# Kernel optimization log

Hardware: AMD Instinct MI355X
Metric: run time of the kernel (lower is better)

## Reference

```python
import jax, jax.numpy as jnp
import numpy as np

B, T, D = 2, 2048, 1024
H = 16
HD = D // H  # head_dim = 64 (kv_rank == embed_dim)
INT4_MIN, INT4_MAX = -8.0, 7.0


def _int4_quant_dequant(x):
    # per-token amax over last dim (head_dim), as in INT4Quantizer with 4-D input
    amax = jnp.max(jnp.abs(x), axis=-1, keepdims=True)
    amax = jnp.maximum(amax, 1e-5)
    scale = amax / 7.0
    q = jnp.clip(jnp.round(x / scale), INT4_MIN, INT4_MAX)  # stored as int8 in cache
    return q * scale


def setup_inputs() -> dict:
    key = jax.random.key(0)
    ks = jax.random.split(key, 11)
    s = 1.0 / np.sqrt(D)
    return {
        "query": jax.random.normal(ks[0], (B, T, D), jnp.float32),
        "key": jax.random.normal(ks[1], (B, T, D), jnp.float32),
        "value": jax.random.normal(ks[2], (B, T, D), jnp.float32),
        "Wq": jax.random.normal(ks[3], (D, D), jnp.float32) * s,
        "bq": jnp.zeros((D,), jnp.float32),
        "Wk": jax.random.normal(ks[4], (D, D), jnp.float32) * s,
        "bk": jnp.zeros((D,), jnp.float32),
        "Wv": jax.random.normal(ks[5], (D, D), jnp.float32) * s,
        "bv": jnp.zeros((D,), jnp.float32),
        "Wo": jax.random.normal(ks[6], (D, D), jnp.float32) * s,
        "bo": jnp.zeros((D,), jnp.float32),
    }


def reference(query, key, value, Wq, bq, Wk, bk, Wv, bv, Wo, bo):
    # projections (nn.Linear: x @ W.T + b)
    q = query @ Wq.T + bq
    k = key @ Wk.T + bk
    v = value @ Wv.T + bv
    # (B, T, D) -> (B, H, T, HD)
    q = q.reshape(B, T, H, HD).transpose(0, 2, 1, 3)
    k = k.reshape(B, T, H, HD).transpose(0, 2, 1, 3)
    v = v.reshape(B, T, H, HD).transpose(0, 2, 1, 3)
    # INT4 quantized KV cache update (use_cache=True): quantize -> scatter into
    # fresh cache -> dequantize the just-written block == quant/dequant of k, v
    k = _int4_quant_dequant(k)
    v = _int4_quant_dequant(v)
    # attention
    scale = HD ** (-0.5)
    attn = jnp.einsum("bhqd,bhkd->bhqk", q, k) * scale
    attn = jax.nn.softmax(attn.astype(jnp.float32), axis=-1).astype(query.dtype)
    out = jnp.einsum("bhqk,bhkd->bhqd", attn, v)
    out = out.transpose(0, 2, 1, 3).reshape(B, T, D)
    out = out @ Wo.T + bo
    return out
```

## Files before the change

### kernel.cpp

```cpp
#include <hip/hip_runtime.h>

typedef unsigned short u16;
typedef unsigned int u32;
typedef float f32x4 __attribute__((ext_vector_type(4)));
typedef float f32x16 __attribute__((ext_vector_type(16)));
typedef short s16x8 __attribute__((ext_vector_type(8)));
typedef u16 u16x8 __attribute__((ext_vector_type(8)));
typedef u16 u16x4 __attribute__((ext_vector_type(4)));
typedef u32 u32x4 __attribute__((ext_vector_type(4)));
typedef _Float16 h16x8 __attribute__((ext_vector_type(8)));
typedef _Float16 h16x2 __attribute__((ext_vector_type(2)));

#define B_ 2
#define T_ 2048
#define H_ 16
#define D_ 1024
#define HD_ 64
#define NTOK (B_*T_)

#define QSCALE 0.18033688011112042f

__device__ __forceinline__ u16 f2b(float f){
  u32 u = __float_as_uint(f);
  return (u16)((u + 0x7fffu + ((u>>16)&1u)) >> 16);
}
__device__ __forceinline__ float b2f(u16 h){ return __uint_as_float(((u32)h)<<16); }

__device__ __forceinline__ void gload_lds16(const u16* g, u16* s){
  __builtin_amdgcn_global_load_lds((const __attribute__((address_space(1))) void*)g,
                                   (__attribute__((address_space(3))) void*)s, 16, 0, 0);
}

template<int ROWS, int WAVES>
__device__ __forceinline__ void stage_tile(const u16* __restrict__ g, size_t ldg,
                                           u16* s, int tid){
  const int w = tid>>6, l = tid&63;
  const int rw = ROWS/WAVES;
  #pragma unroll
  for (int i=0;i<ROWS/(WAVES*8);i++){
    int r0 = w*rw + i*8;
    int r  = r0 + (l>>3);
    int u  = (l&7) ^ (r&7);
    gload_lds16(g + (size_t)r*ldg + (size_t)u*8, s + r0*64);
  }
}

__device__ __forceinline__ u16x8 read_frag(const u16* s, int r, int kk, int l){
  int u = (kk<<2) | (l>>4);
  int phys = u ^ (r&7);
  return *(const u16x8*)(s + r*64 + phys*8);
}
__device__ __forceinline__ u16x8 rfragT(const u16* s, int r, int ks, int hi){
  int phys = (ks*2 + hi) ^ (r&7);
  return *(const u16x8*)(s + r*64 + phys*8);
}

__device__ __forceinline__ void stage_tile32(const u16* __restrict__ g, size_t ldg,
                                             u16* s, int tid){
  const int w = tid>>6, l = tid&63;
  int r0 = w*16;
  int r  = r0 + (l>>2);
  int v  = (l&3) ^ ((r>>1)&3);
  gload_lds16(g + (size_t)r*ldg + (size_t)v*8, s + r0*32);
}
__device__ __forceinline__ u16x8 read_frag32(const u16* s, int r, int l){
  int phys = (l>>4) ^ ((r>>1)&3);
  return *(const u16x8*)(s + r*32 + phys*8);
}

__device__ __forceinline__ f32x4 mfma16_f16(u16x8 a, u16x8 b, f32x4 c){
  return __builtin_amdgcn_mfma_f32_16x16x32_f16(
      __builtin_bit_cast(h16x8,a), __builtin_bit_cast(h16x8,b), c, 0,0,0);
}
__device__ __forceinline__ f32x4 mfma16_bf16(u16x8 a, u16x8 b, f32x4 c){
  return __builtin_amdgcn_mfma_f32_16x16x32_bf16(
      __builtin_bit_cast(s16x8,a), __builtin_bit_cast(s16x8,b), c, 0,0,0);
}
__device__ __forceinline__ f32x16 mfma32_f16(u16x8 a, u16x8 b, f32x16 c){
  return __builtin_amdgcn_mfma_f32_32x32x16_f16(
      __builtin_bit_cast(h16x8,a), __builtin_bit_cast(h16x8,b), c, 0,0,0);
}

__device__ __forceinline__ float ex2(float x){
#if __has_builtin(__builtin_amdgcn_exp2f)
  return __builtin_amdgcn_exp2f(x);
#else
  return exp2f(x);
#endif
}
__device__ __forceinline__ u32 pk2(float a, float b){
  u16 x = __builtin_bit_cast(u16, (_Float16)a);
  u16 y = __builtin_bit_cast(u16, (_Float16)b);
  return (u32)x | ((u32)y<<16);
}
__device__ __forceinline__ u32 pkrtz(float a, float b){
#if __has_builtin(__builtin_amdgcn_cvt_pkrtz)
  auto r = __builtin_amdgcn_cvt_pkrtz(a, b);
  return __builtin_bit_cast(u32, r);
#else
  return pk2(a, b);
#endif
}

__device__ __forceinline__ void split_bf4(const float* in, u16* hi, u16* lo, int i){
  f32x4 v = ((const f32x4*)in)[i];
  u16x4 h, lw;
  #pragma unroll
  for (int j=0;j<4;j++){
    u16 hb = f2b(v[j]);
    h[j] = hb;
    lw[j] = f2b(v[j] - b2f(hb));
  }
  ((u16x4*)hi)[i] = h;
  ((u16x4*)lo)[i] = lw;
}
__device__ __forceinline__ void split_h4(const float* in, u16* out, int i){
  f32x4 v = ((const f32x4*)in)[i];
  u16x4 o;
  #pragma unroll
  for (int j=0;j<4;j++){
    _Float16 t = (_Float16)v[j];
    o[j] = __builtin_bit_cast(u16, t);
  }
  ((u16x4*)out)[i] = o;
}

__global__ void split_inputs_kernel(const float* __restrict__ q, const float* __restrict__ k,
                                    const float* __restrict__ v,
                                    u16* __restrict__ qh, u16* __restrict__ khi, u16* __restrict__ klo,
                                    u16* __restrict__ vhi, u16* __restrict__ vlo){
  int i = blockIdx.x*256 + threadIdx.x;
  int which = blockIdx.y;
  if (which==0)      split_h4 (q, qh, i);
  else if (which==1) split_bf4(k, khi, klo, i);
  else               split_bf4(v, vhi, vlo, i);
}

__global__ void split_weights_kernel(const float* __restrict__ wq, const float* __restrict__ wk,
                                     const float* __restrict__ wv, const float* __restrict__ wo,
                                     u16* __restrict__ wqh, u16* __restrict__ wkh, u16* __restrict__ wkl,
                                     u16* __restrict__ wvh, u16* __restrict__ wvl, u16* __restrict__ woh){
  int i = blockIdx.x*256 + threadIdx.x;
  int which = blockIdx.y;
  if (which==0)      split_h4 (wq, wqh, i);
  else if (which==1) split_bf4(wk, wkh, wkl, i);
  else if (which==2) split_bf4(wv, wvh, wvl, i);
  else               split_h4 (wo, woh, i);
}

template<int F16OUT>
__global__ __launch_bounds__(512)
void gemm1(const u16* __restrict__ Ah, const u16* __restrict__ Wh,
           const float* __restrict__ bias, void* __restrict__ Cout, float oscale)
{
  __shared__ u16 sA[2][128*64];
  __shared__ u16 sW[2][64*64];
  const int tid = threadIdx.x, l = tid&63, l15 = l&15, g = l>>4, w = tid>>6;
  const int wm = w>>1, wn = w&1;
  const int bm = blockIdx.x, bn = blockIdx.y;
  const u16* A0 = Ah + (size_t)bm*128*D_;
  const u16* W0 = Wh + (size_t)bn*64*D_;
  f32x4 acc[2][2] = {};

  stage_tile<128,8>(A0, D_, sA[0], tid);
  stage_tile<64 ,8>(W0, D_, sW[0], tid);
  __syncthreads();
  for (int t=0; t<D_/64; ++t){
    const int cur = t&1;
    if (t+1 < D_/64){
      stage_tile<128,8>(A0 + (t+1)*64, D_, sA[cur^1], tid);
      stage_tile<64 ,8>(W0 + (t+1)*64, D_, sW[cur^1], tid);
    }
    #pragma unroll
    for (int kk=0;kk<2;kk++){
      u16x8 af[2], wf[2];
      #pragma unroll
      for (int fm=0;fm<2;fm++) af[fm] = read_frag(sA[cur], wm*32+fm*16+l15, kk, l);
      #pragma unroll
      for (int fn=0;fn<2;fn++) wf[fn] = read_frag(sW[cur], wn*32+fn*16+l15, kk, l);
      #pragma unroll
      for (int fm=0;fm<2;fm++)
        #pragma unroll
        for (int fn=0;fn<2;fn++)
          acc[fm][fn] = mfma16_f16(af[fm], wf[fn], acc[fm][fn]);
    }
    __syncthreads();
  }

  #pragma unroll
  for (int fn=0; fn<2; fn++){
    int col = bn*64 + wn*32 + fn*16 + l15;
    float bv = bias[col];
    #pragma unroll
    for (int fm=0; fm<2; fm++){
      int r0 = bm*128 + wm*32 + fm*16 + g*4;
      #pragma unroll
      for (int j=0;j<4;j++){
        float v = (acc[fm][fn][j] + bv) * oscale;
        if constexpr (F16OUT){
          ((_Float16*)Cout)[(size_t)(r0+j)*D_ + col] = (_Float16)v;
        } else {
          ((float*)Cout)[(size_t)(r0+j)*D_ + col] = v;
        }
      }
    }
  }
}

template<int QMODE>
__global__ __launch_bounds__(512)
void gemm3_quant(const u16* __restrict__ Ah, const u16* __restrict__ Al,
                 const u16* __restrict__ Wh, const u16* __restrict__ Wl,
                 const float* __restrict__ bias, u16* __restrict__ Out)
{
  extern __shared__ u16 sm[];
  const int tid = threadIdx.x, l = tid&63, w = tid>>6, l15 = l&15, g = l>>4;
  const int wm = w>>1, wn = w&1;
  const int bm = blockIdx.x, bn = blockIdx.y;
  const u16* A0 = Ah + (size_t)bm*128*D_;
  const u16* A1 = Al + (size_t)bm*128*D_;
  const u16* W0 = Wh + (size_t)bn*128*D_;
  const u16* W1 = Wl + (size_t)bn*128*D_;
  constexpr int TS = 128*32;
  f32x4 acc[2][4] = {};

  auto stage = [&](int buf, int t){
    u16* base = sm + buf*4*TS;
    stage_tile32(A0 + t*32, D_, base       , tid);
    stage_tile32(A1 + t*32, D_, base +   TS, tid);
    stage_tile32(W0 + t*32, D_, base + 2*TS, tid);
    stage_tile32(W1 + t*32, D_, base + 3*TS, tid);
  };
  stage(0,0);
  __syncthreads();
  for (int t=0; t<D_/32; ++t){
    const int cur = t&1;
    if (t+1 < D_/32) stage(cur^1, t+1);
    const u16* base = sm + cur*4*TS;
    u16x8 ahh[2], ahl[2], whh[4], whl[4];
    #pragma unroll
    for (int fm=0;fm<2;fm++){
      ahh[fm] = read_frag32(base     , wm*32+fm*16+l15, l);
      ahl[fm] = read_frag32(base+  TS, wm*32+fm*16+l15, l);
    }
    #pragma unroll
    for (int fn=0;fn<4;fn++){
      whh[fn] = read_frag32(base+2*TS, wn*64+fn*16+l15, l);
      whl[fn] = read_frag32(base+3*TS, wn*64+fn*16+l15, l);
    }
    #pragma unroll
    for (int fm=0;fm<2;fm++)
      #pragma unroll
      for (int fn=0;fn<4;fn++){
        acc[fm][fn] = mfma16_bf16(ahh[fm], whh[fn], acc[fm][fn]);
        acc[fm][fn] = mfma16_bf16(ahh[fm], whl[fn], acc[fm][fn]);
        acc[fm][fn] = mfma16_bf16(ahl[fm], whh[fn], acc[fm][fn]);
      }
    __syncthreads();
  }

  #pragma unroll
  for (int fn=0;fn<4;fn++){
    float bv = bias[bn*128 + wn*64 + fn*16 + l15];
    #pragma unroll
    for (int fm=0;fm<2;fm++)
      #pragma unroll
      for (int j=0;j<4;j++) acc[fm][fn][j] += bv;
  }

  u16 (*sdq)[136] = (u16(*)[136])sm;
  #pragma unroll
  for (int fm=0;fm<2;fm++)
    #pragma unroll
    for (int j=0;j<4;j++){
      float a = 0.f;
      #pragma unroll
      for (int fn=0;fn<4;fn++) a = fmaxf(a, fabsf(acc[fm][fn][j]));
      a = fmaxf(a, __shfl_xor(a,1)); a = fmaxf(a, __shfl_xor(a,2));
      a = fmaxf(a, __shfl_xor(a,4)); a = fmaxf(a, __shfl_xor(a,8));
      a = fmaxf(a, 1e-5f);
      float scale = a / 7.0f;
      int row = wm*32 + fm*16 + g*4 + j;
      #pragma unroll
      for (int fn=0;fn<4;fn++){
        float q = rintf(acc[fm][fn][j] / scale);
        q = fminf(fmaxf(q, -8.f), 7.f);
        _Float16 dq = (_Float16)(q * scale);
        int col = wn*64 + fn*16 + l15;
        if (QMODE==1) sdq[row][col] = __builtin_bit_cast(u16, dq);
        else          sdq[col][row] = __builtin_bit_cast(u16, dq);
      }
    }
  __syncthreads();

  if (QMODE==1){
    int r = tid>>2, seg = tid&3;
    u16* dst = Out + (size_t)(bm*128 + r)*D_ + bn*128 + seg*32;
    #pragma unroll
    for (int i=0;i<4;i++)
      *(u16x8*)(dst + i*8) = *(const u16x8*)&sdq[r][seg*32 + i*8];
  } else {
    int cc = tid>>2, seg = tid&3;
    int hh = 2*bn + (cc>>6), dd = cc&63, b = bm>>4;
    u16* dst = Out + ((size_t)((b*H_+hh)*HD_ + dd))*T_ + (bm&15)*128 + seg*32;
    #pragma unroll
    for (int i=0;i<4;i++)
      *(u16x8*)(dst + i*8) = *(const u16x8*)&sdq[cc][seg*32 + i*8];
  }
}

__global__ __launch_bounds__(256, 4)
void attn_kernel(const _Float16* __restrict__ Qp, const u16* __restrict__ Kdq,
                 const u16* __restrict__ Vt, float* __restrict__ po,
                 float* __restrict__ pl)
{
  __shared__ u16 sK[2][64*64];
  __shared__ u16 sV[2][64*64];
  const int tid = threadIdx.x, l = tid&63, c = l&31, hi = l>>5, w = tid>>6;
  const int dsp = blockIdx.x;
  const int xcd = dsp & 7, slot = dsp >> 3;
  const int bh = xcd*4 + (slot>>5);
  const int rem = slot & 31;
  const int qb = rem >> 1, sp = rem & 1;
  const int b = bh>>4, h = bh&15;
  const int off = 4*hi;

  u16x8 qf[4];
  {
    const u16* qrow = (const u16*)Qp + (size_t)(b*T_ + qb*128 + w*32 + c)*D_ + h*HD_;
    #pragma unroll
    for (int ks=0;ks<4;ks++)
      qf[ks] = *(const u16x8*)(qrow + ks*16 + hi*8);
  }

  f32x16 o0 = {}, o1 = {};
  float lsp = 0.f;

  const u16* Kb = Kdq + (size_t)(b*T_ + sp*1024)*D_ + h*HD_;
  const u16* Vb = Vt  + (size_t)(bh*HD_)*T_ + sp*1024;

  stage_tile<64,4>(Kb, D_, sK[0], tid);
  stage_tile<64,4>(Vb, T_, sV[0], tid);
  __syncthreads();

  for (int kt=0; kt<16; kt++){
    const int cur = kt&1;
    if (kt+1 < 16){
      stage_tile<64,4>(Kb + (size_t)((kt+1)*64)*D_, D_, sK[cur^1], tid);
      stage_tile<64,4>(Vb + (kt+1)*64,              T_, sV[cur^1], tid);
    }
    const u16* sKc = sK[cur];
    const u16* sVc = sV[cur];

    #pragma unroll
    for (int kb=0;kb<2;kb++){
      f32x16 s = {};
      #pragma unroll
      for (int ks=0;ks<4;ks++){
        u16x8 kf = rfragT(sKc, kb*32 + c, ks, hi);
        s = mfma32_f16(kf, qf[ks], s);
      }
      u16x8 vfr[2][2];
      #pragma unroll
      for (int vr=0;vr<2;vr++){
        int rv = vr*32 + c;
        int rx = rv & 7;
        const u16* vb = sVc + rv*64 + off;
        #pragma unroll
        for (int part=0;part<2;part++){
          int u0 = 4*kb + 2*part;
          u16x4 lo4 = *(const u16x4*)(vb + ((u0  ) ^ rx)*8);
          u16x4 hi4 = *(const u16x4*)(vb + ((u0+1) ^ rx)*8);
          struct { u16x4 a, b; } t{lo4, hi4};
          vfr[vr][part] = __builtin_bit_cast(u16x8, t);
        }
      }
      float p[16];
      #pragma unroll
      for (int r=0;r<16;r++) p[r] = ex2(s[r]);
      {
        float t0 = (p[0]+p[1]) + (p[2]+p[3]);
        float t1 = (p[4]+p[5]) + (p[6]+p[7]);
        float t2 = (p[8]+p[9]) + (p[10]+p[11]);
        float t3 = (p[12]+p[13]) + (p[14]+p[15]);
        lsp += (t0+t1) + (t2+t3);
      }
      u32x4 pw0 = { pkrtz(p[0],p[1]),  pkrtz(p[2],p[3]),
                    pkrtz(p[4],p[5]),  pkrtz(p[6],p[7]) };
      u32x4 pw1 = { pkrtz(p[8],p[9]),  pkrtz(p[10],p[11]),
                    pkrtz(p[12],p[13]),pkrtz(p[14],p[15]) };
      u16x8 pa0 = __builtin_bit_cast(u16x8, pw0);
      u16x8 pa1 = __builtin_bit_cast(u16x8, pw1);
      o0 = mfma32_f16(pa0, vfr[0][0], o0);
      o0 = mfma32_f16(pa1, vfr[0][1], o0);
      o1 = mfma32_f16(pa0, vfr[1][0], o1);
      o1 = mfma32_f16(pa1, vfr[1][1], o1);
    }
    __syncthreads();
  }

  float lt = lsp + __shfl_xor(lsp, 32);
  if (hi == 0) pl[(size_t)(sp*32 + bh)*T_ + qb*128 + w*32 + c] = lt;

  float* pob = po + ((size_t)(sp*32 + bh)*T_ + qb*128 + w*32)*HD_;
  #pragma unroll
  for (int r=0;r<16;r++){
    int crow = (r&3) + 8*(r>>2) + 4*hi;
    pob[crow*HD_ + c]      = o0[r];
    pob[crow*HD_ + 32 + c] = o1[r];
  }
}

__global__ __launch_bounds__(256)
void combine_kernel(const float* __restrict__ po, const float* __restrict__ pl,
                    u16* __restrict__ Ao)
{
  int i = blockIdx.x*256 + threadIdx.x;
  int d4 = (i & 15) * 4;
  int t  = (i >> 4) & (T_-1);
  int bh = i >> 15;
  size_t r0 = ((size_t)bh*T_ + t);
  f32x4 a = *(const f32x4*)(po + r0*HD_ + d4);
  f32x4 b = *(const f32x4*)(po + (r0 + (size_t)32*T_)*HD_ + d4);
  float lt = pl[r0] + pl[r0 + (size_t)32*T_];
  float rl = 1.0f / lt;
  u16x4 o;
  #pragma unroll
  for (int j=0;j<4;j++)
    o[j] = __builtin_bit_cast(u16, (_Float16)((a[j]+b[j])*rl));
  int bb = bh>>4, hh = bh&15;
  *(u16x4*)(Ao + ((size_t)(bb*T_ + t))*D_ + hh*HD_ + d4) = o;
}

extern "C" void kernel_launch(void* const* d_in, const int* in_sizes, int n_in,
                              void* d_out, int out_size, void* d_ws, size_t ws_size,
                              hipStream_t stream)
{
  (void)in_sizes; (void)n_in; (void)out_size; (void)ws_size;
  const float* query = (const float*)d_in[0];
  const float* key   = (const float*)d_in[1];
  const float* value = (const float*)d_in[2];
  const float* Wq = (const float*)d_in[3];
  const float* bq = (const float*)d_in[4];
  const float* Wk = (const float*)d_in[5];
  const float* bk = (const float*)d_in[6];
  const float* Wv = (const float*)d_in[7];
  const float* bv = (const float*)d_in[8];
  const float* Wo = (const float*)d_in[9];
  const float* bo = (const float*)d_in[10];
  float* out = (float*)d_out;

  char* p = (char*)d_ws;
  auto take = [&](size_t n){ char* r = p; p += (n + 255) & ~(size_t)255; return r; };
  const size_t big = (size_t)NTOK*D_*2;
  const size_t wsz = (size_t)D_*D_*2;

  u16* q_h  = (u16*)take(big);
  u16* khi  = (u16*)take(big);  u16* klo = (u16*)take(big);
  u16* vhi  = (u16*)take(big);  u16* vlo = (u16*)take(big);
  u16* wq_h = (u16*)take(wsz);
  u16* wkh  = (u16*)take(wsz);  u16* wkl = (u16*)take(wsz);
  u16* wvh  = (u16*)take(wsz);  u16* wvl = (u16*)take(wsz);
  u16* wo_h = (u16*)take(wsz);
  u16*  Qp  = (u16*)take(big);
  u16*  Kdq = (u16*)take(big);
  u16*  Vtp = (u16*)take(big);
  u16*  Ao  = (u16*)take(big);

  float* po = (float*)khi;
  float* pl = (float*)wq_h;

  split_inputs_kernel <<<dim3(NTOK*D_/4/256, 3), 256, 0, stream>>>(
      query, key, value, q_h, khi, klo, vhi, vlo);
  split_weights_kernel<<<dim3(D_*D_/4/256, 4), 256, 0, stream>>>(
      Wq, Wk, Wv, Wo, wq_h, wkh, wkl, wvh, wvl, wo_h);

  gemm1<1><<<dim3(32,16), 512, 0, stream>>>(q_h, wq_h, bq, Qp, QSCALE);
  gemm3_quant<1><<<dim3(32,8), 512, 64*1024, stream>>>(khi, klo, wkh, wkl, bk, Kdq);
  gemm3_quant<2><<<dim3(32,8), 512, 64*1024, stream>>>(vhi, vlo, wvh, wvl, bv, Vtp);

  attn_kernel<<<1024, 256, 0, stream>>>((const _Float16*)Qp, Kdq, Vtp, po, pl);
  combine_kernel<<<4096, 256, 0, stream>>>(po, pl, Ao);

  gemm1<0><<<dim3(32,16), 512, 0, stream>>>(Ao, wo_h, bo, out, 1.0f);
}
```

Baseline: 184.4 us.

## Merge split kernels, batch K/V quant GEMMs, retile gemm1 to 32x32 MFMA

Fuses the input and weight split kernels into one launch and runs the K and V quantizing GEMMs as a single launch over a z dimension. gemm1 moves to 128x128 tiles with 4 waves issuing 32x32x16 MFMAs, in place of 16x16 MFMAs on 128x64 tiles with 8 waves. The attention kernel now loads V fragments with the transposed-fragment reader once per tile instead of gathering halves per sub-block, and the V transpose row mapping in the quant epilogue changes to match. The aim is fewer launches, fewer LDS reads and better MFMA throughput, at the cost of fewer blocks for gemm1 and a V layout change that must stay consistent with attention.

```diff
diff --git a/kernel.cpp b/kernel.cpp
--- a/kernel.cpp
+++ b/kernel.cpp
@@ -45,11 +45,6 @@
   }
 }
 
-__device__ __forceinline__ u16x8 read_frag(const u16* s, int r, int kk, int l){
-  int u = (kk<<2) | (l>>4);
-  int phys = u ^ (r&7);
-  return *(const u16x8*)(s + r*64 + phys*8);
-}
 __device__ __forceinline__ u16x8 rfragT(const u16* s, int r, int ks, int hi){
   int phys = (ks*2 + hi) ^ (r&7);
   return *(const u16x8*)(s + r*64 + phys*8);
@@ -68,10 +63,6 @@
   return *(const u16x8*)(s + r*32 + phys*8);
 }
 
-__device__ __forceinline__ f32x4 mfma16_f16(u16x8 a, u16x8 b, f32x4 c){
-  return __builtin_amdgcn_mfma_f32_16x16x32_f16(
-      __builtin_bit_cast(h16x8,a), __builtin_bit_cast(h16x8,b), c, 0,0,0);
-}
 __device__ __forceinline__ f32x4 mfma16_bf16(u16x8 a, u16x8 b, f32x4 c){
   return __builtin_amdgcn_mfma_f32_16x16x32_bf16(
       __builtin_bit_cast(s16x8,a), __builtin_bit_cast(s16x8,b), c, 0,0,0);
@@ -125,98 +116,108 @@
   ((u16x4*)out)[i] = o;
 }
 
-__global__ void split_inputs_kernel(const float* __restrict__ q, const float* __restrict__ k,
-                                    const float* __restrict__ v,
-                                    u16* __restrict__ qh, u16* __restrict__ khi, u16* __restrict__ klo,
-                                    u16* __restrict__ vhi, u16* __restrict__ vlo){
+__global__ void split_all_kernel(const float* __restrict__ q, const float* __restrict__ k,
+                                 const float* __restrict__ v,
+                                 const float* __restrict__ wq, const float* __restrict__ wk,
+                                 const float* __restrict__ wv, const float* __restrict__ wo,
+                                 u16* __restrict__ qh, u16* __restrict__ khi, u16* __restrict__ klo,
+                                 u16* __restrict__ vhi, u16* __restrict__ vlo,
+                                 u16* __restrict__ wqh, u16* __restrict__ wkh, u16* __restrict__ wkl,
+                                 u16* __restrict__ wvh, u16* __restrict__ wvl, u16* __restrict__ woh){
   int i = blockIdx.x*256 + threadIdx.x;
   int which = blockIdx.y;
-  if (which==0)      split_h4 (q, qh, i);
-  else if (which==1) split_bf4(k, khi, klo, i);
-  else               split_bf4(v, vhi, vlo, i);
-}
-
-__global__ void split_weights_kernel(const float* __restrict__ wq, const float* __restrict__ wk,
-                                     const float* __restrict__ wv, const float* __restrict__ wo,
-                                     u16* __restrict__ wqh, u16* __restrict__ wkh, u16* __restrict__ wkl,
-                                     u16* __restrict__ wvh, u16* __restrict__ wvl, u16* __restrict__ woh){
-  int i = blockIdx.x*256 + threadIdx.x;
-  int which = blockIdx.y;
-  if (which==0)      split_h4 (wq, wqh, i);
-  else if (which==1) split_bf4(wk, wkh, wkl, i);
-  else if (which==2) split_bf4(wv, wvh, wvl, i);
-  else               split_h4 (wo, woh, i);
+  if (which < 3){
+    if (which==0)      split_h4 (q, qh, i);
+    else if (which==1) split_bf4(k, khi, klo, i);
+    else               split_bf4(v, vhi, vlo, i);
+  } else {
+    if (i >= D_*D_/4) return;
+    if (which==3)      split_h4 (wq, wqh, i);
+    else if (which==4) split_bf4(wk, wkh, wkl, i);
+    else if (which==5) split_bf4(wv, wvh, wvl, i);
+    else               split_h4 (wo, woh, i);
+  }
 }
 
 template<int F16OUT>
-__global__ __launch_bounds__(512)
+__global__ __launch_bounds__(256)
 void gemm1(const u16* __restrict__ Ah, const u16* __restrict__ Wh,
            const float* __restrict__ bias, void* __restrict__ Cout, float oscale)
 {
   __shared__ u16 sA[2][128*64];
-  __shared__ u16 sW[2][64*64];
-  const int tid = threadIdx.x, l = tid&63, l15 = l&15, g = l>>4, w = tid>>6;
+  __shared__ u16 sW[2][128*64];
+  const int tid = threadIdx.x, l = tid&63, c = l&31, hi = l>>5, w = tid>>6;
   const int wm = w>>1, wn = w&1;
   const int bm = blockIdx.x, bn = blockIdx.y;
   const u16* A0 = Ah + (size_t)bm*128*D_;
-  const u16* W0 = Wh + (size_t)bn*64*D_;
-  f32x4 acc[2][2] = {};
-
-  stage_tile<128,8>(A0, D_, sA[0], tid);
-  stage_tile<64 ,8>(W0, D_, sW[0], tid);
+  const u16* W0 = Wh + (size_t)bn*128*D_;
+  f32x16 acc[2][2] = {};
+
+  stage_tile<128,4>(A0, D_, sA[0], tid);
+  stage_tile<128,4>(W0, D_, sW[0], tid);
   __syncthreads();
   for (int t=0; t<D_/64; ++t){
     const int cur = t&1;
     if (t+1 < D_/64){
-      stage_tile<128,8>(A0 + (t+1)*64, D_, sA[cur^1], tid);
-      stage_tile<64 ,8>(W0 + (t+1)*64, D_, sW[cur^1], tid);
-    }
-    #pragma unroll
-    for (int kk=0;kk<2;kk++){
+      stage_tile<128,4>(A0 + (t+1)*64, D_, sA[cur^1], tid);
+      stage_tile<128,4>(W0 + (t+1)*64, D_, sW[cur^1], tid);
+    }
+    #pragma unroll
+    for (int kc=0;kc<4;kc++){
       u16x8 af[2], wf[2];
-      #pragma unroll
-      for (int fm=0;fm<2;fm++) af[fm] = read_frag(sA[cur], wm*32+fm*16+l15, kk, l);
-      #pragma unroll
-      for (int fn=0;fn<2;fn++) wf[fn] = read_frag(sW[cur], wn*32+fn*16+l15, kk, l);
-      #pragma unroll
-      for (int fm=0;fm<2;fm++)
+      af[0] = rfragT(sA[cur], wm*64 +      c, kc, hi);
+      af[1] = rfragT(sA[cur], wm*64 + 32 + c, kc, hi);
+      wf[0] = rfragT(sW[cur], wn*64 +      c, kc, hi);
+      wf[1] = rfragT(sW[cur], wn*64 + 32 + c, kc, hi);
+      #pragma unroll
+      for (int mb=0;mb<2;mb++)
         #pragma unroll
-        for (int fn=0;fn<2;fn++)
-          acc[fm][fn] = mfma16_f16(af[fm], wf[fn], acc[fm][fn]);
+        for (int nb=0;nb<2;nb++)
+          acc[mb][nb] = mfma32_f16(af[mb], wf[nb], acc[mb][nb]);
     }
     __syncthreads();
   }
 
   #pragma unroll
-  for (int fn=0; fn<2; fn++){
-    int col = bn*64 + wn*32 + fn*16 + l15;
+  for (int nb=0;nb<2;nb++){
+    int col = bn*128 + wn*64 + nb*32 + c;
     float bv = bias[col];
     #pragma unroll
-    for (int fm=0; fm<2; fm++){
-      int r0 = bm*128 + wm*32 + fm*16 + g*4;
-      #pragma unroll
-      for (int j=0;j<4;j++){
-        float v = (acc[fm][fn][j] + bv) * oscale;
+    for (int mb=0;mb<2;mb++){
+      #pragma unroll
+      for (int r=0;r<16;r++){
+        int row = bm*128 + wm*64 + mb*32 + (r&3) + 8*(r>>2) + 4*hi;
+        float v = (acc[mb][nb][r] + bv) * oscale;
         if constexpr (F16OUT){
-          ((_Float16*)Cout)[(size_t)(r0+j)*D_ + col] = (_Float16)v;
+          ((_Float16*)Cout)[(size_t)row*D_ + col] = (_Float16)v;
         } else {
-          ((float*)Cout)[(size_t)(r0+j)*D_ + col] = v;
+          ((float*)Cout)[(size_t)row*D_ + col] = v;
         }
       }
     }
   }
 }
 
-template<int QMODE>
 __global__ __launch_bounds__(512)
-void gemm3_quant(const u16* __restrict__ Ah, const u16* __restrict__ Al,
-                 const u16* __restrict__ Wh, const u16* __restrict__ Wl,
-                 const float* __restrict__ bias, u16* __restrict__ Out)
+void gemm3_quant_kv(const u16* __restrict__ kAh, const u16* __restrict__ kAl,
+                    const u16* __restrict__ kWh, const u16* __restrict__ kWl,
+                    const float* __restrict__ kbias, u16* __restrict__ kOut,
+                    const u16* __restrict__ vAh, const u16* __restrict__ vAl,
+                    const u16* __restrict__ vWh, const u16* __restrict__ vWl,
+                    const float* __restrict__ vbias, u16* __restrict__ vOut)
 {
   extern __shared__ u16 sm[];
   const int tid = threadIdx.x, l = tid&63, w = tid>>6, l15 = l&15, g = l>>4;
   const int wm = w>>1, wn = w&1;
   const int bm = blockIdx.x, bn = blockIdx.y;
+  const bool isV = blockIdx.z != 0;
+  const u16* Ah = isV ? vAh : kAh;
+  const u16* Al = isV ? vAl : kAl;
+  const u16* Wh = isV ? vWh : kWh;
+  const u16* Wl = isV ? vWl : kWl;
+  const float* bias = isV ? vbias : kbias;
+  u16* Out = isV ? vOut : kOut;
+
   const u16* A0 = Ah + (size_t)bm*128*D_;
   const u16* A1 = Al + (size_t)bm*128*D_;
   const u16* W0 = Wh + (size_t)bn*128*D_;
@@ -280,20 +281,22 @@
       a = fmaxf(a, __shfl_xor(a,4)); a = fmaxf(a, __shfl_xor(a,8));
       a = fmaxf(a, 1e-5f);
       float scale = a / 7.0f;
-      int row = wm*32 + fm*16 + g*4 + j;
+      int g2 = ((g&1)<<1) | (g>>1);
+      int rowK = wm*32 + fm*16 + g*4  + j;
+      int rowV = wm*32 + fm*16 + g2*4 + j;
       #pragma unroll
       for (int fn=0;fn<4;fn++){
         float q = rintf(acc[fm][fn][j] / scale);
         q = fminf(fmaxf(q, -8.f), 7.f);
         _Float16 dq = (_Float16)(q * scale);
         int col = wn*64 + fn*16 + l15;
-        if (QMODE==1) sdq[row][col] = __builtin_bit_cast(u16, dq);
-        else          sdq[col][row] = __builtin_bit_cast(u16, dq);
+        if (!isV) sdq[rowK][col] = __builtin_bit_cast(u16, dq);
+        else      sdq[col][rowV] = __builtin_bit_cast(u16, dq);
       }
     }
   __syncthreads();
 
-  if (QMODE==1){
+  if (!isV){
     int r = tid>>2, seg = tid&3;
     u16* dst = Out + (size_t)(bm*128 + r)*D_ + bn*128 + seg*32;
     #pragma unroll
@@ -323,7 +326,6 @@
   const int rem = slot & 31;
   const int qb = rem >> 1, sp = rem & 1;
   const int b = bh>>4, h = bh&15;
-  const int off = 4*hi;
 
   u16x8 qf[4];
   {
@@ -352,6 +354,13 @@
     const u16* sKc = sK[cur];
     const u16* sVc = sV[cur];
 
+    u16x8 vf0[4], vf1[4];
+    #pragma unroll
+    for (int ch=0; ch<4; ch++){
+      vf0[ch] = rfragT(sVc,      c, ch, hi);
+      vf1[ch] = rfragT(sVc, 32 + c, ch, hi);
+    }
+
     #pragma unroll
     for (int kb=0;kb<2;kb++){
       f32x16 s = {};
@@ -359,21 +368,6 @@
       for (int ks=0;ks<4;ks++){
         u16x8 kf = rfragT(sKc, kb*32 + c, ks, hi);
         s = mfma32_f16(kf, qf[ks], s);
-      }
-      u16x8 vfr[2][2];
-      #pragma unroll
-      for (int vr=0;vr<2;vr++){
-        int rv = vr*32 + c;
-        int rx = rv & 7;
-        const u16* vb = sVc + rv*64 + off;
-        #pragma unroll
-        for (int part=0;part<2;part++){
-          int u0 = 4*kb + 2*part;
-          u16x4 lo4 = *(const u16x4*)(vb + ((u0  ) ^ rx)*8);
-          u16x4 hi4 = *(const u16x4*)(vb + ((u0+1) ^ rx)*8);
-          struct { u16x4 a, b; } t{lo4, hi4};
-          vfr[vr][part] = __builtin_bit_cast(u16x8, t);
-        }
       }
       float p[16];
       #pragma unroll
@@ -391,10 +385,10 @@
                     pkrtz(p[12],p[13]),pkrtz(p[14],p[15]) };
       u16x8 pa0 = __builtin_bit_cast(u16x8, pw0);
       u16x8 pa1 = __builtin_bit_cast(u16x8, pw1);
-      o0 = mfma32_f16(pa0, vfr[0][0], o0);
-      o0 = mfma32_f16(pa1, vfr[0][1], o0);
-      o1 = mfma32_f16(pa0, vfr[1][0], o1);
-      o1 = mfma32_f16(pa1, vfr[1][1], o1);
+      o0 = mfma32_f16(pa0, vf0[kb*2+0], o0);
+      o0 = mfma32_f16(pa1, vf0[kb*2+1], o0);
+      o1 = mfma32_f16(pa0, vf1[kb*2+0], o1);
+      o1 = mfma32_f16(pa1, vf1[kb*2+1], o1);
     }
     __syncthreads();
   }
@@ -470,17 +464,19 @@
   float* po = (float*)khi;
   float* pl = (float*)wq_h;
 
-  split_inputs_kernel <<<dim3(NTOK*D_/4/256, 3), 256, 0, stream>>>(
-      query, key, value, q_h, khi, klo, vhi, vlo);
-  split_weights_kernel<<<dim3(D_*D_/4/256, 4), 256, 0, stream>>>(
-      Wq, Wk, Wv, Wo, wq_h, wkh, wkl, wvh, wvl, wo_h);
-
-  gemm1<1><<<dim3(32,16), 512, 0, stream>>>(q_h, wq_h, bq, Qp, QSCALE);
-  gemm3_quant<1><<<dim3(32,8), 512, 64*1024, stream>>>(khi, klo, wkh, wkl, bk, Kdq);
-  gemm3_quant<2><<<dim3(32,8), 512, 64*1024, stream>>>(vhi, vlo, wvh, wvl, bv, Vtp);
+  split_all_kernel<<<dim3(NTOK*D_/4/256, 7), 256, 0, stream>>>(
+      query, key, value, Wq, Wk, Wv, Wo,
+      q_h, khi, klo, vhi, vlo,
+      wq_h, wkh, wkl, wvh, wvl, wo_h);
+
+  gemm1<1><<<dim3(32,8), 256, 0, stream>>>(q_h, wq_h, bq, Qp, QSCALE);
+
+  gemm3_quant_kv<<<dim3(32,8,2), 512, 64*1024, stream>>>(
+      khi, klo, wkh, wkl, bk, Kdq,
+      vhi, vlo, wvh, wvl, bv, Vtp);
 
   attn_kernel<<<1024, 256, 0, stream>>>((const _Float16*)Qp, Kdq, Vtp, po, pl);
   combine_kernel<<<4096, 256, 0, stream>>>(po, pl, Ao);
 
-  gemm1<0><<<dim3(32,16), 512, 0, stream>>>(Ao, wo_h, bo, out, 1.0f);
-}
+  gemm1<0><<<dim3(32,8), 256, 0, stream>>>(Ao, wo_h, bo, out, 1.0f);
+}
```

After: 177.3 us. -3.8%, faster.
